# Optimization experiments

Measured on AMD Instinct MI355X. Metric: run time of the kernel, lower is better.

## Reference

```python
import jax, jax.numpy as jnp
import numpy as np


def setup_inputs() -> dict:
    key = jax.random.key(0)
    B, S, N, D = 4, 512, 8, 256
    ks = jax.random.split(key, 5)
    s = 0.02
    inp = {"x": jax.random.normal(ks[0], (B, S, N, D), jnp.float32)}
    for k, name in zip(ks[1:], ["Wq", "Wk", "Wv", "Wo"]):
        inp[name] = jax.random.normal(k, (D, D), jnp.float32) * s
    for name in ["bq", "bk", "bv", "bo"]:
        inp[name] = jnp.zeros((D,), jnp.float32)
    inp["gamma"] = jnp.ones((D,), jnp.float32)
    inp["beta"] = jnp.zeros((D,), jnp.float32)
    inp["num_heads"] = 8
    return inp


def reference(x, Wq, bq, Wk, bk, Wv, bv, Wo, bo, gamma, beta, num_heads):
    B, S, N, D = x.shape
    H = num_heads
    hd = D // H
    # sinusoidal positional encoding: even dims sin, odd dims cos
    pos = jnp.arange(S, dtype=jnp.float32)[:, None]                      # (S,1)
    div = jnp.exp(jnp.arange(0, D, 2, dtype=jnp.float32) * (-np.log(10000.0) / D))
    ang = pos * div                                                       # (S, D/2)
    pe = jnp.stack([jnp.sin(ang), jnp.cos(ang)], axis=-1).reshape(S, D)   # (S, D)
    x_pos = x + pe[None, :, None, :]                                      # (B,S,N,D)
    # fold sensors into batch: (B*N, S, D)
    xr = x_pos.transpose(0, 2, 1, 3).reshape(B * N, S, D)

    def proj(W, b):
        y = xr @ W.T + b                                                  # torch Linear
        return y.reshape(B * N, S, H, hd).transpose(0, 2, 1, 3)          # (BN,H,S,hd)

    Q, K, V = proj(Wq, bq), proj(Wk, bk), proj(Wv, bv)
    scores = jnp.einsum('bhqd,bhkd->bhqk', Q, K) / np.sqrt(hd)            # (BN,H,S,S)
    causal = jnp.tril(jnp.ones((S, S), dtype=bool))
    scores = jnp.where(causal[None, None], scores, jnp.float32(-1e9))
    attn = jax.nn.softmax(scores, axis=-1)                                # dropout = eval mode
    out = jnp.einsum('bhqk,bhkd->bhqd', attn, V)                          # (BN,H,S,hd)
    out = out.transpose(0, 2, 1, 3).reshape(B * N, S, D)
    out = out @ Wo.T + bo
    out = out.reshape(B, N, S, D).transpose(0, 2, 1, 3)                   # (B,S,N,D)
    y = out + x
    mu = jnp.mean(y, axis=-1, keepdims=True)
    var = jnp.var(y, axis=-1, keepdims=True)
    return (y - mu) / jnp.sqrt(var + 1e-5) * gamma + beta
```

## Files before the change

### kernel.cpp

```cpp
#include <hip/hip_runtime.h>
#include <hip/hip_bf16.h>
#include <math.h>

#define B_   4
#define S_   512
#define N_   8
#define D_   256
#define H_   8
#define HD_  32
#define BN_  32
#define MTOT (BN_ * S_)

typedef __attribute__((ext_vector_type(8))) short short8;
typedef __attribute__((ext_vector_type(4))) short short4v;
typedef __attribute__((ext_vector_type(4))) float floatx4;

#define QSCALE 0.25503468f

__device__ __forceinline__ unsigned short f2bf(float f) {
    union { float f; unsigned u; } c; c.f = f;
    unsigned lsb = (c.u >> 16) & 1u;
    c.u += 0x7fffu + lsb;
    return (unsigned short)(c.u >> 16);
}
__device__ __forceinline__ unsigned short f2bf_ru(float f) {
    union { float f; unsigned u; } c; c.f = f;
    return (unsigned short)((c.u + 0x8000u) >> 16);
}
__device__ __forceinline__ float fexp2(float x) {
    float r; asm("v_exp_f32 %0, %1" : "=v"(r) : "v"(x)); return r;
}

__global__ __launch_bounds__(256) void prep_kernel(const float* __restrict__ x,
                                                   const float* __restrict__ Wq,
                                                   const float* __restrict__ Wk,
                                                   const float* __restrict__ Wv,
                                                   const float* __restrict__ Wo,
                                                   unsigned short* __restrict__ xpos,
                                                   unsigned short* __restrict__ wdst) {
    int bid = blockIdx.x;
    if (bid < 4096) {
        int idx4 = bid * 256 + threadIdx.x;
        int d0 = (idx4 << 2) & (D_ - 1);
        int s  = (idx4 >> 6) & (S_ - 1);
        int bn = idx4 >> 15;
        int b = bn >> 3, n = bn & 7;
        floatx4 xv = *(const floatx4*)(x + ((((size_t)b * S_ + s) * N_ + n) << 8) + d0);
        const float cfreq = -9.210340371976184f / 256.0f;
        float f0 = __expf((float)d0 * cfreq);
        float f1 = __expf((float)(d0 + 2) * cfreq);
        float a0 = (float)s * f0, a1 = (float)s * f1;
        short4v o;
        o[0] = (short)f2bf(xv[0] + __sinf(a0));
        o[1] = (short)f2bf(xv[1] + __cosf(a0));
        o[2] = (short)f2bf(xv[2] + __sinf(a1));
        o[3] = (short)f2bf(xv[3] + __cosf(a1));
        *(short4v*)(xpos + ((size_t)idx4 << 2)) = o;
    } else {
        int idx = (bid - 4096) * 256 + threadIdx.x;
        int which = idx >> 16, off = idx & 65535;
        const float* W = (which == 0) ? Wq : (which == 1) ? Wk : (which == 2) ? Wv : Wo;
        wdst[idx] = f2bf(W[off]);
    }
}

__global__ __launch_bounds__(256) void gemm_qkv_kernel(const unsigned short* __restrict__ A,
                                                       const unsigned short* __restrict__ W,
                                                       const float* __restrict__ bq,
                                                       const float* __restrict__ bk,
                                                       const float* __restrict__ bv,
                                                       unsigned short* __restrict__ Qh,
                                                       unsigned short* __restrict__ Kh,
                                                       unsigned short* __restrict__ Vt) {
    int wv = threadIdx.x >> 6, lane = threadIdx.x & 63;
    int col = lane & 15, quad = lane >> 4;
    int m_w = blockIdx.x * 128 + (wv >> 1) * 64;
    int n_w = blockIdx.y * 128 + (wv & 1) * 64;

    const short8* Ap = (const short8*)(A + (size_t)(m_w + col) * 256 + quad * 8);
    const short8* Bp = (const short8*)(W + (size_t)(n_w + col) * 256 + quad * 8);

    floatx4 acc[4][4] = {};
#pragma unroll
    for (int kk = 0; kk < 8; ++kk) {
        short8 a[4], b[4];
#pragma unroll
        for (int t = 0; t < 4; ++t) {
            a[t] = Ap[t * 512 + kk * 4];
            b[t] = Bp[t * 512 + kk * 4];
        }
#pragma unroll
        for (int mt = 0; mt < 4; ++mt)
#pragma unroll
            for (int nt = 0; nt < 4; ++nt)
                acc[mt][nt] = __builtin_amdgcn_mfma_f32_16x16x32_bf16(a[mt], b[nt], acc[mt][nt], 0, 0, 0);
    }

    int sel = blockIdx.y >> 1;
    const float* bias = (sel == 0) ? bq : (sel == 1) ? bk : bv;
#pragma unroll
    for (int nt = 0; nt < 4; ++nt) {
        int c = n_w + nt * 16 + col - sel * 256;
        float bv_ = bias[c];
#pragma unroll
        for (int mt = 0; mt < 4; ++mt) {
            int m0 = m_w + mt * 16 + quad * 4;
            int bn = m0 >> 9, s0 = m0 & (S_ - 1);
            if (sel == 2) {
                short4v pack;
#pragma unroll
                for (int r = 0; r < 4; ++r) pack[r] = (short)f2bf(acc[mt][nt][r] + bv_);
                *(short4v*)(Vt + (((size_t)((bn << 8) + c)) << 9) + s0) = pack;
            } else {
                int h2 = c >> 5, dl = c & 31;
                unsigned short* dst = ((sel == 0) ? Qh : Kh)
                    + ((((size_t)(bn * 8 + h2)) * 512 + s0) << 5) + dl;
                if (sel == 0) {
#pragma unroll
                    for (int r = 0; r < 4; ++r)
                        dst[r << 5] = f2bf((acc[mt][nt][r] + bv_) * QSCALE);
                } else {
#pragma unroll
                    for (int r = 0; r < 4; ++r)
                        dst[r << 5] = f2bf(acc[mt][nt][r] + bv_);
                }
            }
        }
    }
}

#define PSTR 40
__global__ __launch_bounds__(256) void fattn_kernel(const unsigned short* __restrict__ Qh,
                                                    const unsigned short* __restrict__ Kh,
                                                    const unsigned short* __restrict__ Vt,
                                                    unsigned short* __restrict__ O) {
    __shared__ unsigned short Plds[4][16 * PSTR];
    int wv = threadIdx.x >> 6, lane = threadIdx.x & 63;
    int col = lane & 15, quad = lane >> 4;
    int bnh  = blockIdx.x & 255;
    int qblk = blockIdx.x >> 8;
    int bn = bnh >> 3, h = bnh & 7;
    int q0 = qblk * 64 + wv * 16;

    unsigned short* P = &Plds[wv][0];

    short8 qfrag = *(const short8*)(Qh + (((size_t)(bnh * S_ + q0 + col)) << 5) + quad * 8);
    const unsigned short* Kbase = Kh + (((size_t)(bnh * S_)) << 5) + quad * 8;
    const unsigned short* Vbase = Vt + (((size_t)(bnh * HD_)) << 9) + quad * 8;

    float l = 0.f;
    floatx4 o0 = {0.f, 0.f, 0.f, 0.f};
    floatx4 o1 = {0.f, 0.f, 0.f, 0.f};
    int lastk = q0 >> 5;

    for (int kt = 0; kt <= lastk; ++kt) {
        int k0 = kt * 32;
        short8 kf0 = *(const short8*)(Kbase + ((size_t)(k0 + col) << 5));
        short8 kf1 = *(const short8*)(Kbase + ((size_t)(k0 + 16 + col) << 5));
        floatx4 z = {0.f, 0.f, 0.f, 0.f};
        floatx4 st0 = __builtin_amdgcn_mfma_f32_16x16x32_bf16(kf0, qfrag, z, 0, 0, 0);
        floatx4 st1 = __builtin_amdgcn_mfma_f32_16x16x32_bf16(kf1, qfrag, z, 0, 0, 0);

        if (kt == lastk) {
            int qg = q0 + col;
#pragma unroll
            for (int r = 0; r < 4; ++r) {
                if (k0 + quad * 4 + r > qg)      st0[r] = -1e30f;
                if (k0 + 16 + quad * 4 + r > qg) st1[r] = -1e30f;
            }
        }

        float p[8]; float ts = 0.f;
#pragma unroll
        for (int r = 0; r < 4; ++r) {
            p[r]     = fexp2(st0[r]);
            p[4 + r] = fexp2(st1[r]);
            ts += p[r] + p[4 + r];
        }
        ts += __shfl_xor(ts, 16);
        ts += __shfl_xor(ts, 32);
        l += ts;

        short4v pk0, pk1;
#pragma unroll
        for (int r = 0; r < 4; ++r) {
            pk0[r] = (short)f2bf_ru(p[r]);
            pk1[r] = (short)f2bf_ru(p[4 + r]);
        }
        *(short4v*)&P[col * PSTR + quad * 4]      = pk0;
        *(short4v*)&P[col * PSTR + 16 + quad * 4] = pk1;
        asm volatile("s_waitcnt lgkmcnt(0)" ::: "memory");
        short8 pfrag = *(const short8*)&P[col * PSTR + quad * 8];

        short8 vf0 = *(const short8*)(Vbase + ((size_t)col << 9) + k0);
        short8 vf1 = *(const short8*)(Vbase + ((size_t)(16 + col) << 9) + k0);
        o0 = __builtin_amdgcn_mfma_f32_16x16x32_bf16(vf0, pfrag, o0, 0, 0, 0);
        o1 = __builtin_amdgcn_mfma_f32_16x16x32_bf16(vf1, pfrag, o1, 0, 0, 0);
    }

    float inv = 1.0f / l;
    unsigned short* Op = O + (((size_t)(bn * S_ + q0 + col)) << 8) + h * HD_;
    short4v s0v, s1v;
#pragma unroll
    for (int r = 0; r < 4; ++r) {
        s0v[r] = (short)f2bf(o0[r] * inv);
        s1v[r] = (short)f2bf(o1[r] * inv);
    }
    *(short4v*)(Op + quad * 4)      = s0v;
    *(short4v*)(Op + 16 + quad * 4) = s1v;
}

__global__ __launch_bounds__(256) void gemm_o_ln_kernel(const unsigned short* __restrict__ A,
                                                        const unsigned short* __restrict__ W,
                                                        const float* __restrict__ bo,
                                                        const float* __restrict__ x,
                                                        const float* __restrict__ gamma,
                                                        const float* __restrict__ beta,
                                                        float* __restrict__ out) {
    __shared__ float lsum[4][64];
    __shared__ float lss[4][64];
    __shared__ float lmu[64];
    __shared__ float lrs[64];

    int wv = threadIdx.x >> 6, lane = threadIdx.x & 63;
    int col = lane & 15, quad = lane >> 4;
    int m_b = blockIdx.x * 64;
    int n_w = wv * 64;

    const short8* Ap = (const short8*)(A + (size_t)(m_b + col) * 256 + quad * 8);
    const short8* Bp = (const short8*)(W + (size_t)(n_w + col) * 256 + quad * 8);

    floatx4 acc[4][4] = {};
#pragma unroll
    for (int kk = 0; kk < 8; ++kk) {
        short8 a[4], b[4];
#pragma unroll
        for (int t = 0; t < 4; ++t) {
            a[t] = Ap[t * 512 + kk * 4];
            b[t] = Bp[t * 512 + kk * 4];
        }
#pragma unroll
        for (int mt = 0; mt < 4; ++mt)
#pragma unroll
            for (int nt = 0; nt < 4; ++nt)
                acc[mt][nt] = __builtin_amdgcn_mfma_f32_16x16x32_bf16(a[mt], b[nt], acc[mt][nt], 0, 0, 0);
    }

    int bn = m_b >> 9, s0 = m_b & (S_ - 1);
    int b_ = bn >> 3, n_ = bn & 7;
    const float* xrow = x + ((((size_t)b_ * S_ + s0) * N_ + n_) << 8);
    float* orow = out + ((((size_t)b_ * S_ + s0) * N_ + n_) << 8);

    float psum[4][4] = {};
    float pss[4][4]  = {};
#pragma unroll
    for (int nt = 0; nt < 4; ++nt) {
        int c = n_w + nt * 16 + col;
        float bv_ = bo[c];
#pragma unroll
        for (int mt = 0; mt < 4; ++mt) {
            int sl = mt * 16 + quad * 4;
#pragma unroll
            for (int r = 0; r < 4; ++r) {
                float y = acc[mt][nt][r] + bv_ + xrow[(size_t)(sl + r) * 2048 + c];
                acc[mt][nt][r] = y;
                psum[mt][r] += y;
                pss[mt][r]  += y * y;
            }
        }
    }
#pragma unroll
    for (int off = 8; off >= 1; off >>= 1) {
#pragma unroll
        for (int mt = 0; mt < 4; ++mt)
#pragma unroll
            for (int r = 0; r < 4; ++r) {
                psum[mt][r] += __shfl_xor(psum[mt][r], off);
                pss[mt][r]  += __shfl_xor(pss[mt][r], off);
            }
    }
    if (col == 0) {
#pragma unroll
        for (int mt = 0; mt < 4; ++mt)
#pragma unroll
            for (int r = 0; r < 4; ++r) {
                lsum[wv][mt * 16 + quad * 4 + r] = psum[mt][r];
                lss[wv][mt * 16 + quad * 4 + r]  = pss[mt][r];
            }
    }
    __syncthreads();
    if (threadIdx.x < 64) {
        int row = threadIdx.x;
        float s  = lsum[0][row] + lsum[1][row] + lsum[2][row] + lsum[3][row];
        float ss = lss[0][row] + lss[1][row] + lss[2][row] + lss[3][row];
        float mu = s * (1.0f / 256.0f);
        float var = ss * (1.0f / 256.0f) - mu * mu;
        lmu[row] = mu;
        lrs[row] = rsqrtf(var + 1e-5f);
    }
    __syncthreads();

#pragma unroll
    for (int nt = 0; nt < 4; ++nt) {
        int c = n_w + nt * 16 + col;
        float g  = gamma[c];
        float be = beta[c];
#pragma unroll
        for (int mt = 0; mt < 4; ++mt) {
            int sl = mt * 16 + quad * 4;
#pragma unroll
            for (int r = 0; r < 4; ++r)
                orow[(size_t)(sl + r) * 2048 + c] =
                    (acc[mt][nt][r] - lmu[sl + r]) * lrs[sl + r] * g + be;
        }
    }
}

extern "C" void kernel_launch(void* const* d_in, const int* in_sizes, int n_in,
                              void* d_out, int out_size, void* d_ws, size_t ws_size,
                              hipStream_t stream) {
    const float* x     = (const float*)d_in[0];
    const float* Wq    = (const float*)d_in[1];
    const float* Wk    = (const float*)d_in[2];
    const float* Wv    = (const float*)d_in[3];
    const float* Wo    = (const float*)d_in[4];
    const float* bq    = (const float*)d_in[5];
    const float* bk    = (const float*)d_in[6];
    const float* bv    = (const float*)d_in[7];
    const float* bo    = (const float*)d_in[8];
    const float* gamma = (const float*)d_in[9];
    const float* beta  = (const float*)d_in[10];

    char* w = (char*)d_ws;
    const size_t SZ = (size_t)MTOT * D_ * 2;
    unsigned short* xpos = (unsigned short*)(w);
    unsigned short* Qh   = (unsigned short*)(w + SZ);
    unsigned short* Kh   = (unsigned short*)(w + 2 * SZ);
    unsigned short* Vt   = (unsigned short*)(w + 3 * SZ);
    unsigned short* Ab   = (unsigned short*)(w + 4 * SZ);
    unsigned short* Wbf  = (unsigned short*)(w + 5 * SZ);

    prep_kernel<<<5120, 256, 0, stream>>>(x, Wq, Wk, Wv, Wo, xpos, Wbf);
    gemm_qkv_kernel<<<dim3(128, 6), 256, 0, stream>>>(xpos, Wbf, bq, bk, bv, Qh, Kh, Vt);
    fattn_kernel<<<2048, 256, 0, stream>>>(Qh, Kh, Vt, Ab);
    gemm_o_ln_kernel<<<256, 256, 0, stream>>>(Ab, Wbf + 3 * 65536, bo, x, gamma, beta, (float*)d_out);
}
```

Baseline: 160.8 us.

## Stage full K/V per head in LDS with causal load-balanced query tile pairs

The attention kernel now uses one 1024-thread block per (batch*sensor, head). Each block loads that head's full K and V into padded shared memory once, instead of having 8 query blocks re-read K/V from global memory. Each of the 16 waves handles two query tiles (w and 31-w), so every wave does about the same amount of causal work. The trade-off is only 256 blocks on a large GPU and a sizable LDS footprint per block, which may limit occupancy and leave latency unhidden.

```diff
diff --git a/kernel.cpp b/kernel.cpp
--- a/kernel.cpp
+++ b/kernel.cpp
@@ -129,85 +129,103 @@
     }
 }
 
-#define PSTR 40
-__global__ __launch_bounds__(256) void fattn_kernel(const unsigned short* __restrict__ Qh,
-                                                    const unsigned short* __restrict__ Kh,
-                                                    const unsigned short* __restrict__ Vt,
-                                                    unsigned short* __restrict__ O) {
-    __shared__ unsigned short Plds[4][16 * PSTR];
-    int wv = threadIdx.x >> 6, lane = threadIdx.x & 63;
+#define PSTR  40
+#define KSTR  40
+#define VSTR  520
+__global__ __launch_bounds__(1024) void fattn_kernel(const unsigned short* __restrict__ Qh,
+                                                     const unsigned short* __restrict__ Kh,
+                                                     const unsigned short* __restrict__ Vt,
+                                                     unsigned short* __restrict__ O) {
+    __shared__ unsigned short Klds[S_ * KSTR];
+    __shared__ unsigned short Vlds[HD_ * VSTR];
+    __shared__ unsigned short Plds[16][16 * PSTR];
+
+    int t = threadIdx.x;
+    int bnh = blockIdx.x;
+    int bn = bnh >> 3, h = bnh & 7;
+
+    const unsigned short* Ksrc = Kh + ((size_t)bnh << 14);
+    const unsigned short* Vsrc = Vt + (((size_t)bnh * HD_) << 9);
+#pragma unroll
+    for (int i = 0; i < 2; ++i) {
+        int c = t + i * 1024;
+        int kr = c >> 2, ks = c & 3;
+        *(short8*)&Klds[kr * KSTR + ks * 8] = *(const short8*)(Ksrc + kr * 32 + ks * 8);
+        int vr = c >> 6, vs = c & 63;
+        *(short8*)&Vlds[vr * VSTR + vs * 8] = *(const short8*)(Vsrc + vr * 512 + vs * 8);
+    }
+    __syncthreads();
+
+    int wv = t >> 6, lane = t & 63;
     int col = lane & 15, quad = lane >> 4;
-    int bnh  = blockIdx.x & 255;
-    int qblk = blockIdx.x >> 8;
-    int bn = bnh >> 3, h = bnh & 7;
-    int q0 = qblk * 64 + wv * 16;
-
     unsigned short* P = &Plds[wv][0];
-
-    short8 qfrag = *(const short8*)(Qh + (((size_t)(bnh * S_ + q0 + col)) << 5) + quad * 8);
-    const unsigned short* Kbase = Kh + (((size_t)(bnh * S_)) << 5) + quad * 8;
-    const unsigned short* Vbase = Vt + (((size_t)(bnh * HD_)) << 9) + quad * 8;
-
-    float l = 0.f;
-    floatx4 o0 = {0.f, 0.f, 0.f, 0.f};
-    floatx4 o1 = {0.f, 0.f, 0.f, 0.f};
-    int lastk = q0 >> 5;
-
-    for (int kt = 0; kt <= lastk; ++kt) {
-        int k0 = kt * 32;
-        short8 kf0 = *(const short8*)(Kbase + ((size_t)(k0 + col) << 5));
-        short8 kf1 = *(const short8*)(Kbase + ((size_t)(k0 + 16 + col) << 5));
-        floatx4 z = {0.f, 0.f, 0.f, 0.f};
-        floatx4 st0 = __builtin_amdgcn_mfma_f32_16x16x32_bf16(kf0, qfrag, z, 0, 0, 0);
-        floatx4 st1 = __builtin_amdgcn_mfma_f32_16x16x32_bf16(kf1, qfrag, z, 0, 0, 0);
-
-        if (kt == lastk) {
-            int qg = q0 + col;
-#pragma unroll
-            for (int r = 0; r < 4; ++r) {
-                if (k0 + quad * 4 + r > qg)      st0[r] = -1e30f;
-                if (k0 + 16 + quad * 4 + r > qg) st1[r] = -1e30f;
-            }
-        }
-
-        float p[8]; float ts = 0.f;
+    int qts[2] = { wv, 31 - wv };
+
+#pragma unroll
+    for (int ui = 0; ui < 2; ++ui) {
+        int q0 = qts[ui] * 16;
+        short8 qfrag = *(const short8*)(Qh + (((size_t)(bnh * S_ + q0 + col)) << 5) + quad * 8);
+        float l = 0.f;
+        floatx4 o0 = {0.f, 0.f, 0.f, 0.f};
+        floatx4 o1 = {0.f, 0.f, 0.f, 0.f};
+        int lastk = q0 >> 5;
+
+        for (int kt = 0; kt <= lastk; ++kt) {
+            int k0 = kt * 32;
+            short8 kf0 = *(const short8*)&Klds[(k0 + col) * KSTR + quad * 8];
+            short8 kf1 = *(const short8*)&Klds[(k0 + 16 + col) * KSTR + quad * 8];
+            floatx4 z = {0.f, 0.f, 0.f, 0.f};
+            floatx4 st0 = __builtin_amdgcn_mfma_f32_16x16x32_bf16(kf0, qfrag, z, 0, 0, 0);
+            floatx4 st1 = __builtin_amdgcn_mfma_f32_16x16x32_bf16(kf1, qfrag, z, 0, 0, 0);
+
+            if (kt == lastk) {
+                int qg = q0 + col;
+#pragma unroll
+                for (int r = 0; r < 4; ++r) {
+                    if (k0 + quad * 4 + r > qg)      st0[r] = -1e30f;
+                    if (k0 + 16 + quad * 4 + r > qg) st1[r] = -1e30f;
+                }
+            }
+
+            float p[8]; float ts = 0.f;
+#pragma unroll
+            for (int r = 0; r < 4; ++r) {
+                p[r]     = fexp2(st0[r]);
+                p[4 + r] = fexp2(st1[r]);
+                ts += p[r] + p[4 + r];
+            }
+            ts += __shfl_xor(ts, 16);
+            ts += __shfl_xor(ts, 32);
+            l += ts;
+
+            short4v pk0, pk1;
+#pragma unroll
+            for (int r = 0; r < 4; ++r) {
+                pk0[r] = (short)f2bf_ru(p[r]);
+                pk1[r] = (short)f2bf_ru(p[4 + r]);
+            }
+            *(short4v*)&P[col * PSTR + quad * 4]      = pk0;
+            *(short4v*)&P[col * PSTR + 16 + quad * 4] = pk1;
+            asm volatile("s_waitcnt lgkmcnt(0)" ::: "memory");
+            short8 pfrag = *(const short8*)&P[col * PSTR + quad * 8];
+
+            short8 vf0 = *(const short8*)&Vlds[col * VSTR + k0 + quad * 8];
+            short8 vf1 = *(const short8*)&Vlds[(16 + col) * VSTR + k0 + quad * 8];
+            o0 = __builtin_amdgcn_mfma_f32_16x16x32_bf16(vf0, pfrag, o0, 0, 0, 0);
+            o1 = __builtin_amdgcn_mfma_f32_16x16x32_bf16(vf1, pfrag, o1, 0, 0, 0);
+        }
+
+        float inv = 1.0f / l;
+        unsigned short* Op = O + (((size_t)(bn * S_ + q0 + col)) << 8) + h * HD_;
+        short4v s0v, s1v;
 #pragma unroll
         for (int r = 0; r < 4; ++r) {
-            p[r]     = fexp2(st0[r]);
-            p[4 + r] = fexp2(st1[r]);
-            ts += p[r] + p[4 + r];
-        }
-        ts += __shfl_xor(ts, 16);
-        ts += __shfl_xor(ts, 32);
-        l += ts;
-
-        short4v pk0, pk1;
-#pragma unroll
-        for (int r = 0; r < 4; ++r) {
-            pk0[r] = (short)f2bf_ru(p[r]);
-            pk1[r] = (short)f2bf_ru(p[4 + r]);
-        }
-        *(short4v*)&P[col * PSTR + quad * 4]      = pk0;
-        *(short4v*)&P[col * PSTR + 16 + quad * 4] = pk1;
-        asm volatile("s_waitcnt lgkmcnt(0)" ::: "memory");
-        short8 pfrag = *(const short8*)&P[col * PSTR + quad * 8];
-
-        short8 vf0 = *(const short8*)(Vbase + ((size_t)col << 9) + k0);
-        short8 vf1 = *(const short8*)(Vbase + ((size_t)(16 + col) << 9) + k0);
-        o0 = __builtin_amdgcn_mfma_f32_16x16x32_bf16(vf0, pfrag, o0, 0, 0, 0);
-        o1 = __builtin_amdgcn_mfma_f32_16x16x32_bf16(vf1, pfrag, o1, 0, 0, 0);
-    }
-
-    float inv = 1.0f / l;
-    unsigned short* Op = O + (((size_t)(bn * S_ + q0 + col)) << 8) + h * HD_;
-    short4v s0v, s1v;
-#pragma unroll
-    for (int r = 0; r < 4; ++r) {
-        s0v[r] = (short)f2bf(o0[r] * inv);
-        s1v[r] = (short)f2bf(o1[r] * inv);
-    }
-    *(short4v*)(Op + quad * 4)      = s0v;
-    *(short4v*)(Op + 16 + quad * 4) = s1v;
+            s0v[r] = (short)f2bf(o0[r] * inv);
+            s1v[r] = (short)f2bf(o1[r] * inv);
+        }
+        *(short4v*)(Op + quad * 4)      = s0v;
+        *(short4v*)(Op + 16 + quad * 4) = s1v;
+    }
 }
 
 __global__ __launch_bounds__(256) void gemm_o_ln_kernel(const unsigned short* __restrict__ A,
@@ -342,6 +360,6 @@
 
     prep_kernel<<<5120, 256, 0, stream>>>(x, Wq, Wk, Wv, Wo, xpos, Wbf);
     gemm_qkv_kernel<<<dim3(128, 6), 256, 0, stream>>>(xpos, Wbf, bq, bk, bv, Qh, Kh, Vt);
-    fattn_kernel<<<2048, 256, 0, stream>>>(Qh, Kh, Vt, Ab);
+    fattn_kernel<<<256, 1024, 0, stream>>>(Qh, Kh, Vt, Ab);
     gemm_o_ln_kernel<<<256, 256, 0, stream>>>(Ab, Wbf + 3 * 65536, bo, x, gamma, beta, (float*)d_out);
 }
```

Measured after the change: 149.7 us. 6.9% less time.
